# Performance work log

Hardware: AMD Instinct MI355X
Metric: run time of the kernel (lower is better)

The kernel has to match this reference:

```python
import jax, jax.numpy as jnp
import numpy as np

B, S, F, H = 16, 512, 64, 128          # batch, seq_len, price features, lstm hidden
N, GH = 1024, 64                        # graph nodes, graph hidden
FUSE, H1, H2 = 64, 32, 1                # fusion/output head dims


def setup_inputs() -> dict:
    key = jax.random.key(0)
    ks = jax.random.split(key, 24)
    s = 0.05
    inp = {
        'price_sequence': jax.random.normal(ks[0], (B, S, F), jnp.float32),
        'graph_features': jax.random.normal(ks[1], (B, N, 1), jnp.float32),
        'adjacency_mask': (jax.random.uniform(ks[2], (N, N)) > 0.5).astype(jnp.float32),
        # LSTM layer 0 (torch gate order i,f,g,o; weights stored (4H, in))
        'Wih0': jax.random.normal(ks[3], (4 * H, F), jnp.float32) * s,
        'Whh0': jax.random.normal(ks[4], (4 * H, H), jnp.float32) * s,
        'bih0': jnp.zeros((4 * H,), jnp.float32),
        'bhh0': jnp.zeros((4 * H,), jnp.float32),
        # LSTM layer 1
        'Wih1': jax.random.normal(ks[5], (4 * H, H), jnp.float32) * s,
        'Whh1': jax.random.normal(ks[6], (4 * H, H), jnp.float32) * s,
        'bih1': jnp.zeros((4 * H,), jnp.float32),
        'bhh1': jnp.zeros((4 * H,), jnp.float32),
        # graph attention: W: Linear(1, GH) no bias -> (1, GH); attention Linear(2GH,1) split
        'Wg': jax.random.normal(ks[7], (1, GH), jnp.float32) * s,
        'a_src': jax.random.normal(ks[8], (GH,), jnp.float32) * s,
        'a_dst': jax.random.normal(ks[9], (GH,), jnp.float32) * s,
        'adj_w': jax.random.normal(ks[10], (N, N), jnp.float32) * 0.1,
        # fusion + output head
        'Wf': jax.random.normal(ks[11], (H + N * GH, FUSE), jnp.float32) * 0.01,
        'bf': jnp.zeros((FUSE,), jnp.float32),
        'W1': jax.random.normal(ks[12], (FUSE, H1), jnp.float32) * s,
        'b1': jnp.zeros((H1,), jnp.float32),
        'W2': jax.random.normal(ks[13], (H1, H2), jnp.float32) * s,
        'b2': jnp.zeros((H2,), jnp.float32),
    }
    return inp


def _lstm_layer(x, Wih, Whh, bih, bhh):
    # x: (B, S, in) batch_first; returns (B, S, H)
    b = x.shape[0]
    h0 = jnp.zeros((b, Whh.shape[1]), x.dtype)
    c0 = jnp.zeros_like(h0)
    bias = bih + bhh

    def step(carry, xt):
        h, c = carry
        gates = xt @ Wih.T + h @ Whh.T + bias  # (B, 4H)
        i, f, g, o = jnp.split(gates, 4, axis=-1)
        i, f, o = jax.nn.sigmoid(i), jax.nn.sigmoid(f), jax.nn.sigmoid(o)
        g = jnp.tanh(g)
        c = f * c + i * g
        h = o * jnp.tanh(c)
        return (h, c), h

    _, ys = jax.lax.scan(step, (h0, c0), jnp.swapaxes(x, 0, 1))
    return jnp.swapaxes(ys, 0, 1)


def _graph_attention(graph_features, adjacency_mask, Wg, a_src, a_dst, adj_w):
    h = graph_features @ Wg                       # (B, N, GH)
    # Linear([h_i ; h_j]) == h_i@a_src + h_j@a_dst  (decomposed concat-attention)
    e_src = h @ a_src                              # (B, N)
    e_dst = h @ a_dst                              # (B, N)
    scores = e_src[:, :, None] + e_dst[:, None, :]  # (B, N, N)
    scores = scores * adjacency_mask[None]
    scores = scores * jax.nn.sigmoid(adj_w)[None]
    attn = jax.nn.softmax(scores, axis=-1)
    updated = attn @ h                             # (B, N, GH)
    return updated, attn


def reference(price_sequence, graph_features, adjacency_mask,
              Wih0, Whh0, bih0, bhh0, Wih1, Whh1, bih1, bhh1,
              Wg, a_src, a_dst, adj_w, Wf, bf, W1, b1, W2, b2):
    # 2-layer LSTM (eval mode: inter-layer dropout is identity)
    y0 = _lstm_layer(price_sequence, Wih0, Whh0, bih0, bhh0)
    y1 = _lstm_layer(y0, Wih1, Whh1, bih1, bhh1)
    price_repr = y1[:, -1, :]                      # (B, H)

    graph_repr, attn = _graph_attention(graph_features, adjacency_mask, Wg, a_src, a_dst, adj_w)
    graph_flat = graph_repr.reshape(graph_repr.shape[0], -1)  # (B, N*GH)

    combined = jnp.concatenate([price_repr, graph_flat], axis=1)
    fused = jax.nn.relu(combined @ Wf + bf)
    hidden = jax.nn.relu(fused @ W1 + b1)          # head dropout is identity in eval
    predictions = (hidden @ W2 + b2).squeeze(-1)   # (B,)
    return predictions, attn
```

## Files before the change

kernel.cpp:

```cpp
#include <hip/hip_runtime.h>

typedef unsigned int u32;
typedef unsigned long long u64;
typedef _Float16 f16;
typedef _Float16 f16x8 __attribute__((ext_vector_type(8)));
typedef float f32x4 __attribute__((ext_vector_type(4)));

#define DEV __device__ __forceinline__
#define SCP __HIP_MEMORY_SCOPE_AGENT
#define PINA(x) asm volatile("" : "+a"(x))

constexpr size_t O_XG0   = 0;
constexpr size_t O_W0HI  = O_XG0   + 16ull*512*512*4;
constexpr size_t O_W0LO  = O_W0HI  + 512ull*128*2;
constexpr size_t O_WIHHI = O_W0LO  + 512ull*128*2;
constexpr size_t O_WIHLO = O_WIHHI + 512ull*128*2;
constexpr size_t O_WHHHI = O_WIHLO + 512ull*128*2;
constexpr size_t O_WHHLO = O_WHHHI + 512ull*128*2;
constexpr size_t O_B1P   = O_WHHLO + 512ull*128*2;
constexpr size_t O_MSIG  = O_B1P   + 512*4;
constexpr size_t O_ESC   = O_MSIG  + 1024ull*1024*4;
constexpr size_t O_EDST  = O_ESC   + 16384*4;
constexpr size_t O_SBUF  = O_EDST  + 16384*4;
constexpr size_t O_PREPR = O_SBUF  + 16384*4;
constexpr size_t O_WFG   = O_PREPR + 2048*4;
constexpr size_t O_H0HI  = O_WFG   + 65536ull*4;
constexpr size_t O_H0LO  = O_H0HI  + 513ull*16*64*4;
constexpr size_t O_P1    = O_H0LO  + 513ull*16*64*4;
constexpr size_t O_FLG0  = O_P1    + 513ull*16*512*4;
constexpr size_t O_FLGP  = O_FLG0  + 513ull*16*4;

struct U128 { u64 x, y; };
DEV f16x8 asf16x8(u64 a, u64 b){ U128 t; t.x=a; t.y=b; return __builtin_bit_cast(f16x8, t); }
DEV f32x4 asf32x4(u64 a, u64 b){ U128 t; t.x=a; t.y=b; return __builtin_bit_cast(f32x4, t); }
DEV u32 f16bits(f16 v){ return (u32)__builtin_bit_cast(unsigned short, v); }

DEV float sigm(float x){ x = fminf(fmaxf(x,-30.f),30.f); return __builtin_amdgcn_rcpf(1.f + __expf(-x)); }
DEV float tanh_(float x){ x = fminf(fmaxf(x,-15.f),15.f); float t = __expf(2.f*x); return (t-1.f)*__builtin_amdgcn_rcpf(t+1.f); }

DEV u32 FV(int s){ return 0x5AB00000u + (u32)s; }

DEV void spin1(const u32* p, u32 tv){
  int gd = 1<<20;
  while (__hip_atomic_load(p,__ATOMIC_RELAXED,SCP)!=tv && --gd){}
  (void)__hip_atomic_load(p,__ATOMIC_ACQUIRE,SCP);
}

__global__ __launch_bounds__(256) void k_setup(
    const float* __restrict__ price, const float* __restrict__ gf,
    const float* __restrict__ amask, const float* __restrict__ Wih0,
    const float* __restrict__ Whh0, const float* __restrict__ bih0, const float* __restrict__ bhh0,
    const float* __restrict__ Wih1, const float* __restrict__ Whh1,
    const float* __restrict__ bih1, const float* __restrict__ bhh1,
    const float* __restrict__ Wg, const float* __restrict__ a_src, const float* __restrict__ a_dst,
    const float* __restrict__ adj_w, const float* __restrict__ Wf,
    char* __restrict__ ws)
{
  const int tid = threadIdx.x;
  const int jb = blockIdx.x;
  __shared__ float P[16][64];
  __shared__ float Wt[64][128];

  if (jb < 2048) {
    const int tt = jb >> 2, p0 = (jb & 3) * 128;
    float* XG = (float*)(ws + O_XG0);
    { int idx = tid*4; int b = idx>>6, k = idx&63;
      f32x4 v = *(const f32x4*)(price + ((size_t)b*512 + tt)*64 + k);
      *(f32x4*)&P[b][k] = v; }
    { int c = tid>>1, kh = (tid&1)*32;
      int p = p0 + c; int row = (p&3)*128 + (p>>2);
      const float* src = Wih0 + row*64 + kh;
      #pragma unroll
      for (int kk=0; kk<32; kk+=4){ f32x4 v = *(const f32x4*)(src+kk);
        Wt[kh+kk+0][c]=v[0]; Wt[kh+kk+1][c]=v[1]; Wt[kh+kk+2][c]=v[2]; Wt[kh+kk+3][c]=v[3]; } }
    __syncthreads();
    { int c = tid & 127, hh2 = tid >> 7;
      int p = p0 + c; int row = (p&3)*128 + (p>>2);
      float bias = bih0[row] + bhh0[row];
      float acc[8];
      #pragma unroll
      for (int r2=0;r2<8;r2++) acc[r2] = bias;
      for (int k=0;k<64;k++){ float w = Wt[k][c];
        #pragma unroll
        for (int r2=0;r2<8;r2++) acc[r2] += w * P[hh2*8+r2][k]; }
      #pragma unroll
      for (int r2=0;r2<8;r2++)
        XG[((size_t)(hh2*8+r2)*512 + tt)*512 + p0 + c] = acc[r2]; }
  } else if (jb < 3072) {
    int idx = ((jb-2048)<<10) + tid*4;
    float* MS = (float*)(ws + O_MSIG);
    f32x4 m = *(const f32x4*)(amask+idx); f32x4 a = *(const f32x4*)(adj_w+idx);
    f32x4 o;
    #pragma unroll
    for (int e=0;e<4;e++) o[e] = m[e] * (1.f/(1.f+expf(-a[e])));
    *(f32x4*)(MS+idx) = o;
  } else if (jb < 3136) {
    unsigned short* HI = (unsigned short*)(ws+O_W0HI);
    unsigned short* LO = (unsigned short*)(ws+O_W0LO);
    int base = ((jb-3072)*256 + tid)*4;
    #pragma unroll
    for (int e=0;e<4;e++){ int idx = base+e; int p = idx>>7, k = idx&127;
      int row = (p&3)*128 + (p>>2);
      float w = Whh0[row*128 + k];
      f16 hi = (f16)w; f16 lo = (f16)((w - (float)hi)*4096.f);
      HI[idx] = (unsigned short)f16bits(hi); LO[idx] = (unsigned short)f16bits(lo); }
  } else if (jb < 3200) {
    unsigned short* HI = (unsigned short*)(ws+O_WIHHI);
    unsigned short* LO = (unsigned short*)(ws+O_WIHLO);
    int base = ((jb-3136)*256 + tid)*4;
    #pragma unroll
    for (int e=0;e<4;e++){ int idx = base+e; int p = idx>>7, k = idx&127;
      int row = (p&3)*128 + (p>>2);
      float w = Wih1[row*128 + k];
      f16 hi = (f16)w; f16 lo = (f16)((w - (float)hi)*4096.f);
      HI[idx] = (unsigned short)f16bits(hi); LO[idx] = (unsigned short)f16bits(lo); }
  } else if (jb < 3264) {
    unsigned short* HI = (unsigned short*)(ws+O_WHHHI);
    unsigned short* LO = (unsigned short*)(ws+O_WHHLO);
    int base = ((jb-3200)*256 + tid)*4;
    #pragma unroll
    for (int e=0;e<4;e++){ int idx = base+e; int p = idx>>7, k = idx&127;
      int row = (p&3)*128 + (p>>2);
      float w = Whh1[row*128 + k];
      f16 hi = (f16)w; f16 lo = (f16)((w - (float)hi)*4096.f);
      HI[idx] = (unsigned short)f16bits(hi); LO[idx] = (unsigned short)f16bits(lo); }
  } else if (jb < 3265) {
    float* B1 = (float*)(ws+O_B1P);
    for (int p = tid; p < 512; p += 256){ int row = (p&3)*128 + (p>>2); B1[p] = bih1[row]+bhh1[row]; }
  } else if (jb < 3281) {
    float cs = 0.f, cd = 0.f;
    for (int g=0; g<64; g++){ cs += Wg[g]*a_src[g]; cd += Wg[g]*a_dst[g]; }
    float* ESC = (float*)(ws+O_ESC); float* EDS = (float*)(ws+O_EDST);
    int base = (jb-3265)*1024 + tid*4;
    f32x4 g4 = *(const f32x4*)(gf+base);
    f32x4 e1, e2;
    #pragma unroll
    for (int e=0;e<4;e++){ e1[e] = g4[e]*cs; e2[e] = g4[e]*cd; }
    *(f32x4*)(ESC+base) = e1; *(f32x4*)(EDS+base) = e2;
  } else {
    float* WFG = (float*)(ws+O_WFG);
    int n = (jb-3281)*4 + (tid>>6); int f = tid & 63;
    float acc = 0.f;
    for (int g=0; g<64; g++) acc += Wg[g] * Wf[((size_t)(128 + n*64 + g))*64 + f];
    WFG[n*64 + f] = acc;
  }
}

struct SM {
  u32 hHI[2][64];
  u32 hLO[2][64];
  float gbuf[8][64];
  float red[8];
};

template<int LAYER>
DEV void rnn_cu(char* __restrict__ ws, int b, int tid, SM* sm)
{
  const int lane = tid & 63, w = tid >> 6;
  const int c = lane & 15, q = lane >> 4;
  const int j = w*16 + c;

  const u64* WHI = (const u64*)(ws + (LAYER ? O_WHHHI : O_W0HI));
  const u64* WLO = (const u64*)(ws + (LAYER ? O_WHHLO : O_W0LO));
  f16x8 Bhi[4][4], Blo[4][4];
  #pragma unroll
  for (int t=0;t<4;t++)
    #pragma unroll
    for (int ks=0;ks<4;ks++){
      int o = (w*64 + t*16 + c)*32 + ks*8 + q*2;
      Bhi[t][ks] = asf16x8(WHI[o], WHI[o+1]);
      Blo[t][ks] = asf16x8(WLO[o], WLO[o+1]);
    }
  #pragma unroll
  for (int t=0;t<4;t++)
    #pragma unroll
    for (int ks=0;ks<4;ks++){ PINA(Bhi[t][ks]); PINA(Blo[t][ks]); }

  u32* H0HIp = (u32*)(ws+O_H0HI);
  u32* H0LOp = (u32*)(ws+O_H0LO);
  const u64* P1u = (const u64*)(ws+O_P1);
  const u32* FLGPp = (const u32*)(ws+O_FLGP);
  u32* FLG0p = (u32*)(ws+O_FLG0);
  const float* XGb = (const float*)(ws+O_XG0) + (size_t)b*512*512;

  if (q==0 && (c&1)==0){ sm->hHI[0][w*8+(c>>1)] = 0u; sm->hLO[0][w*8+(c>>1)] = 0u; }

  f32x4 xgc = {0,0,0,0}, xgN = {0,0,0,0}, xgNN = {0,0,0,0};
  u64 pc0=0, pc1=0, pn0=0, pn1=0, pnn0=0, pnn1=0;
  if constexpr (!LAYER) {
    xgc = *(const f32x4*)(XGb + 4*j);
    xgN = *(const f32x4*)(XGb + 512 + 4*j);
    xgNN = xgN;
  } else {
    spin1(FLGPp + 1, FV(1));
    { size_t o = ((size_t)(1*16 + b)*512 + 4*j) >> 1;
      pc0 = __hip_atomic_load(P1u+o,   __ATOMIC_RELAXED, SCP);
      pc1 = __hip_atomic_load(P1u+o+1, __ATOMIC_RELAXED, SCP); }
    spin1(FLGPp + 2, FV(2));
    { size_t o = ((size_t)(2*16 + b)*512 + 4*j) >> 1;
      pn0 = __hip_atomic_load(P1u+o,   __ATOMIC_RELAXED, SCP);
      pn1 = __hip_atomic_load(P1u+o+1, __ATOMIC_RELAXED, SCP); }
  }
  u32 huP=0, luP=0;
  float cst = 0.f;
  __syncthreads();
  int cur = 0;

  for (int s=1; s<=512; ++s){
    if constexpr (!LAYER) {
      if (s>=2 && q==0 && (c&1)==0){
        int o = ((s-1)*16 + b)*64 + w*8 + (c>>1);
        __hip_atomic_store(H0HIp+o, huP, __ATOMIC_RELAXED, SCP);
        __hip_atomic_store(H0LOp+o, luP, __ATOMIC_RELAXED, SCP);
      }
      if (s <= 510) xgNN = *(const f32x4*)(XGb + (size_t)(s+1)*512 + 4*j);
    }

    f32x4 acc[4], accl[4];
    #pragma unroll
    for (int t=0;t<4;t++){ acc[t]=f32x4{0,0,0,0}; accl[t]=f32x4{0,0,0,0}; }
    #pragma unroll
    for (int ks=0;ks<4;ks++){
      f16x8 ah  = *(const f16x8*)&sm->hHI[cur][ks*16 + q*4];
      f16x8 al_ = *(const f16x8*)&sm->hLO[cur][ks*16 + q*4];
      #pragma unroll
      for (int t=0;t<4;t++){
        acc[t]  = __builtin_amdgcn_mfma_f32_16x16x32_f16(ah,  Bhi[t][ks], acc[t],  0,0,0);
        accl[t] = __builtin_amdgcn_mfma_f32_16x16x32_f16(ah,  Blo[t][ks], accl[t], 0,0,0);
        accl[t] = __builtin_amdgcn_mfma_f32_16x16x32_f16(al_, Bhi[t][ks], accl[t], 0,0,0);
      }
    }

    if constexpr (LAYER) {
      if (s+2 <= 512){
        spin1(FLGPp + (s+2), FV(s+2));
        size_t o = ((size_t)((s+2)*16 + b)*512 + 4*j) >> 1;
        pnn0 = __hip_atomic_load(P1u+o,   __ATOMIC_RELAXED, SCP);
        pnn1 = __hip_atomic_load(P1u+o+1, __ATOMIC_RELAXED, SCP);
      }
    }

    if (q==0){
      #pragma unroll
      for (int t=0;t<4;t++) sm->gbuf[w][t*16+c] = acc[t][0] + accl[t][0]*(1.f/4096.f);
    }
    f32x4 g4 = *(const f32x4*)&sm->gbuf[w][4*c];
    f32x4 add = LAYER ? asf32x4(pc0,pc1) : xgc;
    float I = sigm(g4[0]+add[0]);
    float F = sigm(g4[1]+add[1]);
    float G = tanh_(g4[2]+add[2]);
    float O = sigm(g4[3]+add[3]);
    cst = F*cst + I*G;
    float hv = O * tanh_(cst);

    f16 hh = (f16)hv; f16 hl = (f16)((hv - (float)hh)*4096.f);
    u32 hb = f16bits(hh), lb = f16bits(hl);
    u32 oh = (u32)__shfl_xor((int)hb, 1, 64);
    u32 ol = (u32)__shfl_xor((int)lb, 1, 64);
    u32 hu = hb | (oh<<16), lu = lb | (ol<<16);
    int nxt = cur^1;
    if (q==0 && (c&1)==0){ sm->hHI[nxt][w*8+(c>>1)] = hu; sm->hLO[nxt][w*8+(c>>1)] = lu; }
    if constexpr (LAYER){ if (s==512 && q==0) ((float*)(ws+O_PREPR))[b*128 + j] = hv; }

    if constexpr (!LAYER){ asm volatile("s_waitcnt vmcnt(0)" ::: "memory"); }
    __syncthreads();
    if constexpr (!LAYER){
      if (s>=2 && tid==0)
        __hip_atomic_store(FLG0p + (s-1)*16 + b, FV(s-1), __ATOMIC_RELAXED, SCP);
    }
    huP=hu; luP=lu; cur = nxt;
    xgc = xgN; xgN = xgNN;
    pc0=pn0; pc1=pn1; pn0=pnn0; pn1=pnn1;
  }

  if constexpr (!LAYER){
    if (q==0 && (c&1)==0){
      int o = (512*16 + b)*64 + w*8 + (c>>1);
      __hip_atomic_store(H0HIp+o, huP, __ATOMIC_RELAXED, SCP);
      __hip_atomic_store(H0LOp+o, luP, __ATOMIC_RELAXED, SCP);
    }
    asm volatile("s_waitcnt vmcnt(0)" ::: "memory");
    __syncthreads();
    if (tid==0) __hip_atomic_store(FLG0p + 512*16 + b, FV(512), __ATOMIC_RELAXED, SCP);
  }
}

DEV void gemm_cu(char* __restrict__ ws, int g, int tid)
{
  const int lane = tid & 63, w = tid >> 6;
  const int c = lane & 15, q = lane >> 4;

  const u64* WHI = (const u64*)(ws+O_WIHHI);
  const u64* WLO = (const u64*)(ws+O_WIHLO);
  f16x8 Bhi[4][4], Blo[4][4];
  #pragma unroll
  for (int t=0;t<4;t++)
    #pragma unroll
    for (int ks=0;ks<4;ks++){
      int o = (w*64 + t*16 + c)*32 + ks*8 + q*2;
      Bhi[t][ks] = asf16x8(WHI[o], WHI[o+1]);
      Blo[t][ks] = asf16x8(WLO[o], WLO[o+1]);
    }
  #pragma unroll
  for (int t=0;t<4;t++)
    #pragma unroll
    for (int ks=0;ks<4;ks++){ PINA(Bhi[t][ks]); PINA(Blo[t][ks]); }

  float bias_t[4];
  #pragma unroll
  for (int t=0;t<4;t++) bias_t[t] = ((const float*)(ws+O_B1P))[w*64 + t*16 + c];

  const u64* H0HIu = (const u64*)(ws+O_H0HI);
  const u64* H0LOu = (const u64*)(ws+O_H0LO);
  const u32* FLG0p = (const u32*)(ws+O_FLG0);
  u32* FLGPp = (u32*)(ws+O_FLGP);
  float* P1f = (float*)(ws+O_P1);

  for (int s = 1+g; s <= 512; s += 3){
    { const u32* fp = FLG0p + s*16 + c; int gd = 1<<20; u32 tv = FV(s);
      for(;;){ bool ok = (lane>=16) || (__hip_atomic_load(fp,__ATOMIC_RELAXED,SCP)==tv);
               if (__all(ok) || !--gd) break; }
      (void)__hip_atomic_load(fp, __ATOMIC_ACQUIRE, SCP); }

    u64 AH[4][2], AL[4][2];
    #pragma unroll
    for (int ks=0;ks<4;ks++){
      size_t o = ((size_t)(s*16 + c))*32 + ks*8 + q*2;
      AH[ks][0]=__hip_atomic_load(H0HIu+o,  __ATOMIC_RELAXED,SCP);
      AH[ks][1]=__hip_atomic_load(H0HIu+o+1,__ATOMIC_RELAXED,SCP);
      AL[ks][0]=__hip_atomic_load(H0LOu+o,  __ATOMIC_RELAXED,SCP);
      AL[ks][1]=__hip_atomic_load(H0LOu+o+1,__ATOMIC_RELAXED,SCP);
    }
    f32x4 acc[4], accl[4];
    #pragma unroll
    for (int t=0;t<4;t++){ acc[t]=f32x4{0,0,0,0}; accl[t]=f32x4{0,0,0,0}; }
    #pragma unroll
    for (int ks=0;ks<4;ks++){
      f16x8 ah  = asf16x8(AH[ks][0], AH[ks][1]);
      f16x8 al_ = asf16x8(AL[ks][0], AL[ks][1]);
      #pragma unroll
      for (int t=0;t<4;t++){
        acc[t]  = __builtin_amdgcn_mfma_f32_16x16x32_f16(ah,  Bhi[t][ks], acc[t],  0,0,0);
        accl[t] = __builtin_amdgcn_mfma_f32_16x16x32_f16(ah,  Blo[t][ks], accl[t], 0,0,0);
        accl[t] = __builtin_amdgcn_mfma_f32_16x16x32_f16(al_, Bhi[t][ks], accl[t], 0,0,0);
      }
    }
    #pragma unroll
    for (int t=0;t<4;t++){
      #pragma unroll
      for (int i=0;i<4;i++){
        float v = acc[t][i] + accl[t][i]*(1.f/4096.f) + bias_t[t];
        __hip_atomic_store(P1f + ((size_t)(s*16 + q*4 + i))*512 + w*64 + t*16 + c,
                           v, __ATOMIC_RELAXED, SCP);
      }
    }
    asm volatile("s_waitcnt vmcnt(0)" ::: "memory");
    __syncthreads();
    if (tid==0) __hip_atomic_store(FLGPp + s, FV(s), __ATOMIC_RELAXED, SCP);
  }
}

DEV float wredMax(float v){
  #pragma unroll
  for (int o=32;o;o>>=1) v = fmaxf(v, __shfl_xor(v,o,64));
  return v;
}
DEV float wredSum(float v){
  #pragma unroll
  for (int o=32;o;o>>=1) v += __shfl_xor(v,o,64);
  return v;
}

__global__
__attribute__((amdgpu_flat_work_group_size(512,512), amdgpu_waves_per_eu(2,2)))
void k_main(const float* __restrict__ gf, char* __restrict__ ws, float* __restrict__ out)
{
  __shared__ SM sm;
  const int tid = threadIdx.x;
  const int bid = blockIdx.x;

  if (bid < 16) { rnn_cu<0>(ws, bid, tid, &sm); return; }
  if (bid < 32) { rnn_cu<1>(ws, bid-16, tid, &sm); return; }
  if (bid < 35) { gemm_cu(ws, bid-32, tid); return; }

  const int row = bid - 35;
  const int b = row >> 10, i = row & 1023;
  const int w = tid >> 6;
  const float* MSIG = (const float*)(ws+O_MSIG);
  const float* ESC  = (const float*)(ws+O_ESC);
  const float* EDST = (const float*)(ws+O_EDST);
  float* SBUF = (float*)(ws+O_SBUF);

  const float ei = ESC[(b<<10)+i];
  float pv[2];
  float mx = -3.4e38f;
  #pragma unroll
  for (int k2=0;k2<2;k2++){
    int jj = tid + (k2<<9);
    float sc = (ei + EDST[(b<<10)+jj]) * MSIG[((size_t)i<<10)+jj];
    pv[k2] = sc; mx = fmaxf(mx, sc);
  }
  mx = wredMax(mx);
  if ((tid&63)==0) sm.red[w] = mx;
  __syncthreads();
  mx = fmaxf(fmaxf(fmaxf(sm.red[0],sm.red[1]),fmaxf(sm.red[2],sm.red[3])),
             fmaxf(fmaxf(sm.red[4],sm.red[5]),fmaxf(sm.red[6],sm.red[7])));
  __syncthreads();

  float sum = 0.f;
  #pragma unroll
  for (int k2=0;k2<2;k2++){ pv[k2] = __expf(pv[k2]-mx); sum += pv[k2]; }
  sum = wredSum(sum);
  if ((tid&63)==0) sm.red[w] = sum;
  __syncthreads();
  sum = sm.red[0]+sm.red[1]+sm.red[2]+sm.red[3]+sm.red[4]+sm.red[5]+sm.red[6]+sm.red[7];
  __syncthreads();

  const float rinv = 1.0f / sum;
  float sacc = 0.f;
  const size_t obase = 16 + ((size_t)row << 10);
  #pragma unroll
  for (int k2=0;k2<2;k2++){
    int jj = tid + (k2<<9);
    float a = pv[k2]*rinv;
    out[obase + jj] = a;
    sacc += a * gf[(b<<10)+jj];
  }
  sacc = wredSum(sacc);
  if ((tid&63)==0) sm.red[w] = sacc;
  __syncthreads();
  if (tid==0) SBUF[row] = sm.red[0]+sm.red[1]+sm.red[2]+sm.red[3]
                        + sm.red[4]+sm.red[5]+sm.red[6]+sm.red[7];
}

__global__ __launch_bounds__(256) void k_mlp(const float* __restrict__ Wf, const float* __restrict__ bf,
  const float* __restrict__ W1, const float* __restrict__ b1,
  const float* __restrict__ W2, const float* __restrict__ b2,
  const char* __restrict__ ws, float* __restrict__ out)
{
  __shared__ float sS[1024];
  __shared__ float sP[128];
  __shared__ float sR[256];
  __shared__ float sF[96];
  const int b = blockIdx.x, tid = threadIdx.x;
  const float* SBUF = (const float*)(ws+O_SBUF);
  const float* PREPR= (const float*)(ws+O_PREPR);
  const float* WFG  = (const float*)(ws+O_WFG);

  { f32x4 v = *(const f32x4*)(SBUF + (b<<10) + tid*4); *(f32x4*)&sS[tid*4] = v; }
  if (tid < 128) sP[tid] = PREPR[b*128 + tid];
  __syncthreads();

  const int f = tid & 63, kq = tid >> 6;
  float acc = 0.f;
  for (int n = kq*256; n < kq*256+256; ++n) acc += sS[n] * WFG[n*64 + f];
  if (kq == 0) {
    for (int k=0;k<128;k++) acc += sP[k] * Wf[k*64 + f];
    acc += bf[f];
  }
  sR[tid] = acc; __syncthreads();
  if (tid < 64) {
    float v = sR[tid] + sR[tid+64] + sR[tid+128] + sR[tid+192];
    sF[tid] = fmaxf(v, 0.f);
  }
  __syncthreads();
  if (tid < 32) {
    float a = 0.f;
    for (int k=0;k<64;k++) a += sF[k] * W1[k*32 + tid];
    sF[64+tid] = fmaxf(a + b1[tid], 0.f);
  }
  __syncthreads();
  if (tid == 0) {
    float a = 0.f;
    for (int k=0;k<32;k++) a += sF[64+k] * W2[k];
    out[b] = a + b2[0];
  }
}

extern "C" void kernel_launch(void* const* d_in, const int* in_sizes, int n_in,
                              void* d_out, int out_size, void* d_ws, size_t ws_size,
                              hipStream_t stream)
{
  const float* price = (const float*)d_in[0];
  const float* gf    = (const float*)d_in[1];
  const float* amask = (const float*)d_in[2];
  const float* Wih0  = (const float*)d_in[3];
  const float* Whh0  = (const float*)d_in[4];
  const float* bih0  = (const float*)d_in[5];
  const float* bhh0  = (const float*)d_in[6];
  const float* Wih1  = (const float*)d_in[7];
  const float* Whh1  = (const float*)d_in[8];
  const float* bih1  = (const float*)d_in[9];
  const float* bhh1  = (const float*)d_in[10];
  const float* Wg    = (const float*)d_in[11];
  const float* asrc  = (const float*)d_in[12];
  const float* adst  = (const float*)d_in[13];
  const float* adjw  = (const float*)d_in[14];
  const float* Wf    = (const float*)d_in[15];
  const float* bf    = (const float*)d_in[16];
  const float* W1    = (const float*)d_in[17];
  const float* b1    = (const float*)d_in[18];
  const float* W2    = (const float*)d_in[19];
  const float* b2    = (const float*)d_in[20];
  char* ws = (char*)d_ws;
  float* out = (float*)d_out;

  k_setup<<<dim3(3537), dim3(256), 0, stream>>>(price, gf, amask, Wih0, Whh0, bih0, bhh0,
                                                Wih1, Whh1, bih1, bhh1, Wg, asrc, adst, adjw, Wf, ws);
  k_main<<<dim3(35 + 16384), dim3(512), 0, stream>>>(gf, ws, out);
  k_mlp<<<dim3(16), dim3(256), 0, stream>>>(Wf, bf, W1, b1, W2, b2, (const char*)ws, out);
}
```

Baseline: 1.205 ms.

## Replace flag-synchronized LSTM layer pipeline with separate sequential kernel launches

Splits the single persistent kernel into separate launches: layer-0 recurrence plus attention rows, a batched input-projection GEMM over all timesteps, then the layer-1 recurrence. This removes the global flag spinning and the per-step vmcnt waits, and uses an LDS-only barrier in the recurrent loop. The cost is that the two recurrences no longer overlap, so their serial step chains add up.

```diff
diff --git a/kernel.cpp b/kernel.cpp
--- a/kernel.cpp
+++ b/kernel.cpp
@@ -27,8 +27,6 @@
 constexpr size_t O_H0HI  = O_WFG   + 65536ull*4;
 constexpr size_t O_H0LO  = O_H0HI  + 513ull*16*64*4;
 constexpr size_t O_P1    = O_H0LO  + 513ull*16*64*4;
-constexpr size_t O_FLG0  = O_P1    + 513ull*16*512*4;
-constexpr size_t O_FLGP  = O_FLG0  + 513ull*16*4;
 
 struct U128 { u64 x, y; };
 DEV f16x8 asf16x8(u64 a, u64 b){ U128 t; t.x=a; t.y=b; return __builtin_bit_cast(f16x8, t); }
@@ -38,12 +36,10 @@
 DEV float sigm(float x){ x = fminf(fmaxf(x,-30.f),30.f); return __builtin_amdgcn_rcpf(1.f + __expf(-x)); }
 DEV float tanh_(float x){ x = fminf(fmaxf(x,-15.f),15.f); float t = __expf(2.f*x); return (t-1.f)*__builtin_amdgcn_rcpf(t+1.f); }
 
-DEV u32 FV(int s){ return 0x5AB00000u + (u32)s; }
-
-DEV void spin1(const u32* p, u32 tv){
-  int gd = 1<<20;
-  while (__hip_atomic_load(p,__ATOMIC_RELAXED,SCP)!=tv && --gd){}
-  (void)__hip_atomic_load(p,__ATOMIC_ACQUIRE,SCP);
+DEV void bar_lds(){
+  asm volatile("s_waitcnt lgkmcnt(0)" ::: "memory");
+  __builtin_amdgcn_s_barrier();
+  __builtin_amdgcn_sched_barrier(0);
 }
 
 __global__ __launch_bounds__(256) void k_setup(
@@ -154,7 +150,7 @@
 };
 
 template<int LAYER>
-DEV void rnn_cu(char* __restrict__ ws, int b, int tid, SM* sm)
+DEV void rnn_seq(char* __restrict__ ws, int b, int tid, SM* sm)
 {
   const int lane = tid & 63, w = tid >> 6;
   const int c = lane & 15, q = lane >> 4;
@@ -179,8 +175,6 @@
   u32* H0HIp = (u32*)(ws+O_H0HI);
   u32* H0LOp = (u32*)(ws+O_H0LO);
   const u64* P1u = (const u64*)(ws+O_P1);
-  const u32* FLGPp = (const u32*)(ws+O_FLGP);
-  u32* FLG0p = (u32*)(ws+O_FLG0);
   const float* XGb = (const float*)(ws+O_XG0) + (size_t)b*512*512;
 
   if (q==0 && (c&1)==0){ sm->hHI[0][w*8+(c>>1)] = 0u; sm->hLO[0][w*8+(c>>1)] = 0u; }
@@ -190,21 +184,18 @@
   if constexpr (!LAYER) {
     xgc = *(const f32x4*)(XGb + 4*j);
     xgN = *(const f32x4*)(XGb + 512 + 4*j);
-    xgNN = xgN;
   } else {
-    spin1(FLGPp + 1, FV(1));
     { size_t o = ((size_t)(1*16 + b)*512 + 4*j) >> 1;
       pc0 = __hip_atomic_load(P1u+o,   __ATOMIC_RELAXED, SCP);
       pc1 = __hip_atomic_load(P1u+o+1, __ATOMIC_RELAXED, SCP); }
-    spin1(FLGPp + 2, FV(2));
     { size_t o = ((size_t)(2*16 + b)*512 + 4*j) >> 1;
       pn0 = __hip_atomic_load(P1u+o,   __ATOMIC_RELAXED, SCP);
       pn1 = __hip_atomic_load(P1u+o+1, __ATOMIC_RELAXED, SCP); }
   }
   u32 huP=0, luP=0;
   float cst = 0.f;
-  __syncthreads();
   int cur = 0;
+  __syncthreads();
 
   for (int s=1; s<=512; ++s){
     if constexpr (!LAYER) {
@@ -214,6 +205,12 @@
         __hip_atomic_store(H0LOp+o, luP, __ATOMIC_RELAXED, SCP);
       }
       if (s <= 510) xgNN = *(const f32x4*)(XGb + (size_t)(s+1)*512 + 4*j);
+    } else {
+      if (s+2 <= 512){
+        size_t o = ((size_t)((s+2)*16 + b)*512 + 4*j) >> 1;
+        pnn0 = __hip_atomic_load(P1u+o,   __ATOMIC_RELAXED, SCP);
+        pnn1 = __hip_atomic_load(P1u+o+1, __ATOMIC_RELAXED, SCP);
+      }
     }
 
     f32x4 acc[4], accl[4];
@@ -231,15 +228,6 @@
       }
     }
 
-    if constexpr (LAYER) {
-      if (s+2 <= 512){
-        spin1(FLGPp + (s+2), FV(s+2));
-        size_t o = ((size_t)((s+2)*16 + b)*512 + 4*j) >> 1;
-        pnn0 = __hip_atomic_load(P1u+o,   __ATOMIC_RELAXED, SCP);
-        pnn1 = __hip_atomic_load(P1u+o+1, __ATOMIC_RELAXED, SCP);
-      }
-    }
-
     if (q==0){
       #pragma unroll
       for (int t=0;t<4;t++) sm->gbuf[w][t*16+c] = acc[t][0] + accl[t][0]*(1.f/4096.f);
@@ -262,12 +250,8 @@
     if (q==0 && (c&1)==0){ sm->hHI[nxt][w*8+(c>>1)] = hu; sm->hLO[nxt][w*8+(c>>1)] = lu; }
     if constexpr (LAYER){ if (s==512 && q==0) ((float*)(ws+O_PREPR))[b*128 + j] = hv; }
 
-    if constexpr (!LAYER){ asm volatile("s_waitcnt vmcnt(0)" ::: "memory"); }
-    __syncthreads();
-    if constexpr (!LAYER){
-      if (s>=2 && tid==0)
-        __hip_atomic_store(FLG0p + (s-1)*16 + b, FV(s-1), __ATOMIC_RELAXED, SCP);
-    }
+    bar_lds();
+
     huP=hu; luP=lu; cur = nxt;
     xgc = xgN; xgN = xgNN;
     pc0=pn0; pc1=pn1; pn0=pnn0; pn1=pnn1;
@@ -279,84 +263,6 @@
       __hip_atomic_store(H0HIp+o, huP, __ATOMIC_RELAXED, SCP);
       __hip_atomic_store(H0LOp+o, luP, __ATOMIC_RELAXED, SCP);
     }
-    asm volatile("s_waitcnt vmcnt(0)" ::: "memory");
-    __syncthreads();
-    if (tid==0) __hip_atomic_store(FLG0p + 512*16 + b, FV(512), __ATOMIC_RELAXED, SCP);
-  }
-}
-
-DEV void gemm_cu(char* __restrict__ ws, int g, int tid)
-{
-  const int lane = tid & 63, w = tid >> 6;
-  const int c = lane & 15, q = lane >> 4;
-
-  const u64* WHI = (const u64*)(ws+O_WIHHI);
-  const u64* WLO = (const u64*)(ws+O_WIHLO);
-  f16x8 Bhi[4][4], Blo[4][4];
-  #pragma unroll
-  for (int t=0;t<4;t++)
-    #pragma unroll
-    for (int ks=0;ks<4;ks++){
-      int o = (w*64 + t*16 + c)*32 + ks*8 + q*2;
-      Bhi[t][ks] = asf16x8(WHI[o], WHI[o+1]);
-      Blo[t][ks] = asf16x8(WLO[o], WLO[o+1]);
-    }
-  #pragma unroll
-  for (int t=0;t<4;t++)
-    #pragma unroll
-    for (int ks=0;ks<4;ks++){ PINA(Bhi[t][ks]); PINA(Blo[t][ks]); }
-
-  float bias_t[4];
-  #pragma unroll
-  for (int t=0;t<4;t++) bias_t[t] = ((const float*)(ws+O_B1P))[w*64 + t*16 + c];
-
-  const u64* H0HIu = (const u64*)(ws+O_H0HI);
-  const u64* H0LOu = (const u64*)(ws+O_H0LO);
-  const u32* FLG0p = (const u32*)(ws+O_FLG0);
-  u32* FLGPp = (u32*)(ws+O_FLGP);
-  float* P1f = (float*)(ws+O_P1);
-
-  for (int s = 1+g; s <= 512; s += 3){
-    { const u32* fp = FLG0p + s*16 + c; int gd = 1<<20; u32 tv = FV(s);
-      for(;;){ bool ok = (lane>=16) || (__hip_atomic_load(fp,__ATOMIC_RELAXED,SCP)==tv);
-               if (__all(ok) || !--gd) break; }
-      (void)__hip_atomic_load(fp, __ATOMIC_ACQUIRE, SCP); }
-
-    u64 AH[4][2], AL[4][2];
-    #pragma unroll
-    for (int ks=0;ks<4;ks++){
-      size_t o = ((size_t)(s*16 + c))*32 + ks*8 + q*2;
-      AH[ks][0]=__hip_atomic_load(H0HIu+o,  __ATOMIC_RELAXED,SCP);
-      AH[ks][1]=__hip_atomic_load(H0HIu+o+1,__ATOMIC_RELAXED,SCP);
-      AL[ks][0]=__hip_atomic_load(H0LOu+o,  __ATOMIC_RELAXED,SCP);
-      AL[ks][1]=__hip_atomic_load(H0LOu+o+1,__ATOMIC_RELAXED,SCP);
-    }
-    f32x4 acc[4], accl[4];
-    #pragma unroll
-    for (int t=0;t<4;t++){ acc[t]=f32x4{0,0,0,0}; accl[t]=f32x4{0,0,0,0}; }
-    #pragma unroll
-    for (int ks=0;ks<4;ks++){
-      f16x8 ah  = asf16x8(AH[ks][0], AH[ks][1]);
-      f16x8 al_ = asf16x8(AL[ks][0], AL[ks][1]);
-      #pragma unroll
-      for (int t=0;t<4;t++){
-        acc[t]  = __builtin_amdgcn_mfma_f32_16x16x32_f16(ah,  Bhi[t][ks], acc[t],  0,0,0);
-        accl[t] = __builtin_amdgcn_mfma_f32_16x16x32_f16(ah,  Blo[t][ks], accl[t], 0,0,0);
-        accl[t] = __builtin_amdgcn_mfma_f32_16x16x32_f16(al_, Bhi[t][ks], accl[t], 0,0,0);
-      }
-    }
-    #pragma unroll
-    for (int t=0;t<4;t++){
-      #pragma unroll
-      for (int i=0;i<4;i++){
-        float v = acc[t][i] + accl[t][i]*(1.f/4096.f) + bias_t[t];
-        __hip_atomic_store(P1f + ((size_t)(s*16 + q*4 + i))*512 + w*64 + t*16 + c,
-                           v, __ATOMIC_RELAXED, SCP);
-      }
-    }
-    asm volatile("s_waitcnt vmcnt(0)" ::: "memory");
-    __syncthreads();
-    if (tid==0) __hip_atomic_store(FLGPp + s, FV(s), __ATOMIC_RELAXED, SCP);
   }
 }
 
@@ -373,17 +279,15 @@
 
 __global__
 __attribute__((amdgpu_flat_work_group_size(512,512), amdgpu_waves_per_eu(2,2)))
-void k_main(const float* __restrict__ gf, char* __restrict__ ws, float* __restrict__ out)
+void k_lstm0(const float* __restrict__ gf, char* __restrict__ ws, float* __restrict__ out)
 {
   __shared__ SM sm;
   const int tid = threadIdx.x;
   const int bid = blockIdx.x;
 
-  if (bid < 16) { rnn_cu<0>(ws, bid, tid, &sm); return; }
-  if (bid < 32) { rnn_cu<1>(ws, bid-16, tid, &sm); return; }
-  if (bid < 35) { gemm_cu(ws, bid-32, tid); return; }
-
-  const int row = bid - 35;
+  if (bid < 16) { rnn_seq<0>(ws, bid, tid, &sm); return; }
+
+  const int row = bid - 16;
   const int b = row >> 10, i = row & 1023;
   const int w = tid >> 6;
   const float* MSIG = (const float*)(ws+O_MSIG);
@@ -431,6 +335,75 @@
   __syncthreads();
   if (tid==0) SBUF[row] = sm.red[0]+sm.red[1]+sm.red[2]+sm.red[3]
                         + sm.red[4]+sm.red[5]+sm.red[6]+sm.red[7];
+}
+
+__global__
+__attribute__((amdgpu_flat_work_group_size(512,512), amdgpu_waves_per_eu(2,2)))
+void k_gemm1(char* __restrict__ ws)
+{
+  const int tid = threadIdx.x;
+  const int lane = tid & 63, w = tid >> 6;
+  const int c = lane & 15, q = lane >> 4;
+  const int s = blockIdx.x + 1;
+
+  const u64* WHI = (const u64*)(ws+O_WIHHI);
+  const u64* WLO = (const u64*)(ws+O_WIHLO);
+  f16x8 Bhi[4][4], Blo[4][4];
+  #pragma unroll
+  for (int t=0;t<4;t++)
+    #pragma unroll
+    for (int ks=0;ks<4;ks++){
+      int o = (w*64 + t*16 + c)*32 + ks*8 + q*2;
+      Bhi[t][ks] = asf16x8(WHI[o], WHI[o+1]);
+      Blo[t][ks] = asf16x8(WLO[o], WLO[o+1]);
+    }
+  float bias_t[4];
+  #pragma unroll
+  for (int t=0;t<4;t++) bias_t[t] = ((const float*)(ws+O_B1P))[w*64 + t*16 + c];
+
+  const u64* H0HIu = (const u64*)(ws+O_H0HI);
+  const u64* H0LOu = (const u64*)(ws+O_H0LO);
+  float* P1f = (float*)(ws+O_P1);
+
+  u64 AH[4][2], AL[4][2];
+  #pragma unroll
+  for (int ks=0;ks<4;ks++){
+    size_t o = ((size_t)(s*16 + c))*32 + ks*8 + q*2;
+    AH[ks][0]=__hip_atomic_load(H0HIu+o,  __ATOMIC_RELAXED,SCP);
+    AH[ks][1]=__hip_atomic_load(H0HIu+o+1,__ATOMIC_RELAXED,SCP);
+    AL[ks][0]=__hip_atomic_load(H0LOu+o,  __ATOMIC_RELAXED,SCP);
+    AL[ks][1]=__hip_atomic_load(H0LOu+o+1,__ATOMIC_RELAXED,SCP);
+  }
+  f32x4 acc[4], accl[4];
+  #pragma unroll
+  for (int t=0;t<4;t++){ acc[t]=f32x4{0,0,0,0}; accl[t]=f32x4{0,0,0,0}; }
+  #pragma unroll
+  for (int ks=0;ks<4;ks++){
+    f16x8 ah  = asf16x8(AH[ks][0], AH[ks][1]);
+    f16x8 al_ = asf16x8(AL[ks][0], AL[ks][1]);
+    #pragma unroll
+    for (int t=0;t<4;t++){
+      acc[t]  = __builtin_amdgcn_mfma_f32_16x16x32_f16(ah,  Bhi[t][ks], acc[t],  0,0,0);
+      accl[t] = __builtin_amdgcn_mfma_f32_16x16x32_f16(ah,  Blo[t][ks], accl[t], 0,0,0);
+      accl[t] = __builtin_amdgcn_mfma_f32_16x16x32_f16(al_, Bhi[t][ks], accl[t], 0,0,0);
+    }
+  }
+  #pragma unroll
+  for (int t=0;t<4;t++){
+    #pragma unroll
+    for (int i=0;i<4;i++){
+      float v = acc[t][i] + accl[t][i]*(1.f/4096.f) + bias_t[t];
+      P1f[((size_t)(s*16 + q*4 + i))*512 + w*64 + t*16 + c] = v;
+    }
+  }
+}
+
+__global__
+__attribute__((amdgpu_flat_work_group_size(512,512), amdgpu_waves_per_eu(2,2)))
+void k_lstm1(char* __restrict__ ws)
+{
+  __shared__ SM sm;
+  rnn_seq<1>(ws, blockIdx.x, threadIdx.x, &sm);
 }
 
 __global__ __launch_bounds__(256) void k_mlp(const float* __restrict__ Wf, const float* __restrict__ bf,
@@ -507,6 +480,8 @@
 
   k_setup<<<dim3(3537), dim3(256), 0, stream>>>(price, gf, amask, Wih0, Whh0, bih0, bhh0,
                                                 Wih1, Whh1, bih1, bhh1, Wg, asrc, adst, adjw, Wf, ws);
-  k_main<<<dim3(35 + 16384), dim3(512), 0, stream>>>(gf, ws, out);
+  k_lstm0<<<dim3(16 + 16384), dim3(512), 0, stream>>>(gf, ws, out);
+  k_gemm1<<<dim3(512), dim3(512), 0, stream>>>(ws);
+  k_lstm1<<<dim3(16), dim3(512), 0, stream>>>(ws);
   k_mlp<<<dim3(16), dim3(256), 0, stream>>>(Wf, bf, W1, b1, W2, b2, (const char*)ws, out);
 }
```

Result: slower. 1.554 ms (+28.9%).

## Batch eight sequences per recurrent workgroup and split attention into its own kernel

Applied to the files above, without the earlier changes.

The recurrent LSTM workgroups now each handle eight batch rows instead of one, using the MFMA M dimension (hi and lo f16 halves of h stacked as 16 rows), so only 2+2 recurrent blocks run instead of 16+16. Gate outputs are regathered through a padded LDS transpose, and the error-correction term uses a cross-lane shuffle. The graph-attention rows move into a separate kernel launched after the recurrent one, and the flag layout changes to per-group strides. This cuts per-step MFMA waste and barrier count per sequence, but each block does more serial work per step and attention no longer overlaps with the recurrence.

```diff
diff --git a/kernel.cpp b/kernel.cpp
--- a/kernel.cpp
+++ b/kernel.cpp
@@ -32,7 +32,6 @@
 
 struct U128 { u64 x, y; };
 DEV f16x8 asf16x8(u64 a, u64 b){ U128 t; t.x=a; t.y=b; return __builtin_bit_cast(f16x8, t); }
-DEV f32x4 asf32x4(u64 a, u64 b){ U128 t; t.x=a; t.y=b; return __builtin_bit_cast(f32x4, t); }
 DEV u32 f16bits(f16 v){ return (u32)__builtin_bit_cast(unsigned short, v); }
 
 DEV float sigm(float x){ x = fminf(fmaxf(x,-30.f),30.f); return __builtin_amdgcn_rcpf(1.f + __expf(-x)); }
@@ -44,6 +43,17 @@
   int gd = 1<<20;
   while (__hip_atomic_load(p,__ATOMIC_RELAXED,SCP)!=tv && --gd){}
   (void)__hip_atomic_load(p,__ATOMIC_ACQUIRE,SCP);
+}
+
+DEV void bar_lds(){
+  asm volatile("s_waitcnt lgkmcnt(0)" ::: "memory");
+  __builtin_amdgcn_s_barrier();
+  __builtin_amdgcn_sched_barrier(0);
+}
+DEV void bar_vm2(){
+  asm volatile("s_waitcnt vmcnt(2) lgkmcnt(0)" ::: "memory");
+  __builtin_amdgcn_s_barrier();
+  __builtin_amdgcn_sched_barrier(0);
 }
 
 __global__ __launch_bounds__(256) void k_setup(
@@ -146,19 +156,18 @@
   }
 }
 
-struct SM {
-  u32 hHI[2][64];
-  u32 hLO[2][64];
-  float gbuf[8][64];
-  float red[8];
+struct SM2 {
+  u32 hbuf[2][16][72];
+  float gbuf[8][585];
 };
 
 template<int LAYER>
-DEV void rnn_cu(char* __restrict__ ws, int b, int tid, SM* sm)
+DEV void rnn2(char* __restrict__ ws, int bg, int tid, SM2* sm)
 {
   const int lane = tid & 63, w = tid >> 6;
-  const int c = lane & 15, q = lane >> 4;
-  const int j = w*16 + c;
+  const int r = lane & 15, q = lane >> 4;
+  const int b_loc = lane >> 3, jl0 = lane & 7;
+  const int B = bg*8 + b_loc;
 
   const u64* WHI = (const u64*)(ws + (LAYER ? O_WHHHI : O_W0HI));
   const u64* WLO = (const u64*)(ws + (LAYER ? O_WHHLO : O_W0LO));
@@ -167,7 +176,7 @@
   for (int t=0;t<4;t++)
     #pragma unroll
     for (int ks=0;ks<4;ks++){
-      int o = (w*64 + t*16 + c)*32 + ks*8 + q*2;
+      int o = (w*64 + t*16 + r)*32 + ks*8 + q*2;
       Bhi[t][ks] = asf16x8(WHI[o], WHI[o+1]);
       Blo[t][ks] = asf16x8(WLO[o], WLO[o+1]);
     }
@@ -178,110 +187,174 @@
 
   u32* H0HIp = (u32*)(ws+O_H0HI);
   u32* H0LOp = (u32*)(ws+O_H0LO);
-  const u64* P1u = (const u64*)(ws+O_P1);
+  const float* P1f = (const float*)(ws+O_P1);
   const u32* FLGPp = (const u32*)(ws+O_FLGP);
   u32* FLG0p = (u32*)(ws+O_FLG0);
-  const float* XGb = (const float*)(ws+O_XG0) + (size_t)b*512*512;
-
-  if (q==0 && (c&1)==0){ sm->hHI[0][w*8+(c>>1)] = 0u; sm->hLO[0][w*8+(c>>1)] = 0u; }
-
-  f32x4 xgc = {0,0,0,0}, xgN = {0,0,0,0}, xgNN = {0,0,0,0};
-  u64 pc0=0, pc1=0, pn0=0, pn1=0, pnn0=0, pnn1=0;
+  const float* XGb = (const float*)(ws+O_XG0) + (size_t)B*512*512;
+
+  for (int idx = tid; idx < 2*16*72; idx += 512) ((u32*)sm->hbuf)[idx] = 0u;
+
+  f32x4 xgc[2], xgN[2], xgNN[2];
+  f32x4 p1c[2], p1n[2], p1nn[2];
+  #pragma unroll
+  for (int g2=0; g2<2; ++g2){ xgc[g2]=f32x4{0,0,0,0}; xgN[g2]=f32x4{0,0,0,0}; xgNN[g2]=f32x4{0,0,0,0};
+                              p1c[g2]=f32x4{0,0,0,0}; p1n[g2]=f32x4{0,0,0,0}; p1nn[g2]=f32x4{0,0,0,0}; }
   if constexpr (!LAYER) {
-    xgc = *(const f32x4*)(XGb + 4*j);
-    xgN = *(const f32x4*)(XGb + 512 + 4*j);
-    xgNN = xgN;
+    #pragma unroll
+    for (int g2=0; g2<2; ++g2){
+      int jg = 16*w + 8*g2 + jl0;
+      xgc[g2] = *(const f32x4*)(XGb + 4*jg);
+      xgN[g2] = *(const f32x4*)(XGb + 512 + 4*jg);
+    }
   } else {
-    spin1(FLGPp + 1, FV(1));
-    { size_t o = ((size_t)(1*16 + b)*512 + 4*j) >> 1;
-      pc0 = __hip_atomic_load(P1u+o,   __ATOMIC_RELAXED, SCP);
-      pc1 = __hip_atomic_load(P1u+o+1, __ATOMIC_RELAXED, SCP); }
-    spin1(FLGPp + 2, FV(2));
-    { size_t o = ((size_t)(2*16 + b)*512 + 4*j) >> 1;
-      pn0 = __hip_atomic_load(P1u+o,   __ATOMIC_RELAXED, SCP);
-      pn1 = __hip_atomic_load(P1u+o+1, __ATOMIC_RELAXED, SCP); }
-  }
-  u32 huP=0, luP=0;
-  float cst = 0.f;
-  __syncthreads();
+    spin1(FLGPp + 1*16, FV(1));
+    #pragma unroll
+    for (int g2=0; g2<2; ++g2){
+      int jg = 16*w + 8*g2 + jl0;
+      p1c[g2] = *(const f32x4*)(P1f + ((size_t)(1*16 + B))*512 + 4*jg);
+    }
+    spin1(FLGPp + 2*16, FV(2));
+    #pragma unroll
+    for (int g2=0; g2<2; ++g2){
+      int jg = 16*w + 8*g2 + jl0;
+      p1n[g2] = *(const f32x4*)(P1f + ((size_t)(2*16 + B))*512 + 4*jg);
+    }
+  }
+  u32 huP[2] = {0,0}, luP[2] = {0,0};
+  float cst[2] = {0.f, 0.f};
   int cur = 0;
+  __syncthreads();
 
   for (int s=1; s<=512; ++s){
     if constexpr (!LAYER) {
-      if (s>=2 && q==0 && (c&1)==0){
-        int o = ((s-1)*16 + b)*64 + w*8 + (c>>1);
-        __hip_atomic_store(H0HIp+o, huP, __ATOMIC_RELAXED, SCP);
-        __hip_atomic_store(H0LOp+o, luP, __ATOMIC_RELAXED, SCP);
-      }
-      if (s <= 510) xgNN = *(const f32x4*)(XGb + (size_t)(s+1)*512 + 4*j);
-    }
-
-    f32x4 acc[4], accl[4];
-    #pragma unroll
-    for (int t=0;t<4;t++){ acc[t]=f32x4{0,0,0,0}; accl[t]=f32x4{0,0,0,0}; }
+      if (s>=2 && (jl0&1)==0){
+        #pragma unroll
+        for (int g2=0; g2<2; ++g2){
+          int o = ((s-1)*16 + B)*64 + 8*w + 4*g2 + (jl0>>1);
+          __hip_atomic_store(H0HIp+o, huP[g2], __ATOMIC_RELAXED, SCP);
+          __hip_atomic_store(H0LOp+o, luP[g2], __ATOMIC_RELAXED, SCP);
+        }
+      }
+      __builtin_amdgcn_sched_barrier(0);
+      { int rowN = (s<=510) ? (s+1) : 511;
+        #pragma unroll
+        for (int g2=0; g2<2; ++g2){
+          int jg = 16*w + 8*g2 + jl0;
+          xgNN[g2] = *(const f32x4*)(XGb + (size_t)rowN*512 + 4*jg);
+        } }
+    }
+
+    f32x4 accA[4], accB[4];
+    #pragma unroll
+    for (int t=0;t<4;t++){ accA[t]=f32x4{0,0,0,0}; accB[t]=f32x4{0,0,0,0}; }
     #pragma unroll
     for (int ks=0;ks<4;ks++){
-      f16x8 ah  = *(const f16x8*)&sm->hHI[cur][ks*16 + q*4];
-      f16x8 al_ = *(const f16x8*)&sm->hLO[cur][ks*16 + q*4];
+      f16x8 av = *(const f16x8*)&sm->hbuf[cur][r][ks*16 + q*4];
       #pragma unroll
       for (int t=0;t<4;t++){
-        acc[t]  = __builtin_amdgcn_mfma_f32_16x16x32_f16(ah,  Bhi[t][ks], acc[t],  0,0,0);
-        accl[t] = __builtin_amdgcn_mfma_f32_16x16x32_f16(ah,  Blo[t][ks], accl[t], 0,0,0);
-        accl[t] = __builtin_amdgcn_mfma_f32_16x16x32_f16(al_, Bhi[t][ks], accl[t], 0,0,0);
+        accA[t] = __builtin_amdgcn_mfma_f32_16x16x32_f16(av, Bhi[t][ks], accA[t], 0,0,0);
+        accB[t] = __builtin_amdgcn_mfma_f32_16x16x32_f16(av, Blo[t][ks], accB[t], 0,0,0);
       }
     }
 
     if constexpr (LAYER) {
       if (s+2 <= 512){
-        spin1(FLGPp + (s+2), FV(s+2));
-        size_t o = ((size_t)((s+2)*16 + b)*512 + 4*j) >> 1;
-        pnn0 = __hip_atomic_load(P1u+o,   __ATOMIC_RELAXED, SCP);
-        pnn1 = __hip_atomic_load(P1u+o+1, __ATOMIC_RELAXED, SCP);
-      }
-    }
-
-    if (q==0){
-      #pragma unroll
-      for (int t=0;t<4;t++) sm->gbuf[w][t*16+c] = acc[t][0] + accl[t][0]*(1.f/4096.f);
-    }
-    f32x4 g4 = *(const f32x4*)&sm->gbuf[w][4*c];
-    f32x4 add = LAYER ? asf32x4(pc0,pc1) : xgc;
-    float I = sigm(g4[0]+add[0]);
-    float F = sigm(g4[1]+add[1]);
-    float G = tanh_(g4[2]+add[2]);
-    float O = sigm(g4[3]+add[3]);
-    cst = F*cst + I*G;
-    float hv = O * tanh_(cst);
-
-    f16 hh = (f16)hv; f16 hl = (f16)((hv - (float)hh)*4096.f);
-    u32 hb = f16bits(hh), lb = f16bits(hl);
-    u32 oh = (u32)__shfl_xor((int)hb, 1, 64);
-    u32 ol = (u32)__shfl_xor((int)lb, 1, 64);
-    u32 hu = hb | (oh<<16), lu = lb | (ol<<16);
+        spin1(FLGPp + (s+2)*16, FV(s+2));
+        #pragma unroll
+        for (int g2=0; g2<2; ++g2){
+          int jg = 16*w + 8*g2 + jl0;
+          p1nn[g2] = *(const f32x4*)(P1f + ((size_t)((s+2)*16 + B))*512 + 4*jg);
+        }
+      }
+    }
+
+    f32x4 gate_t[4];
+    #pragma unroll
+    for (int t=0;t<4;t++){
+      #pragma unroll
+      for (int i=0;i<4;i++){
+        float corr = __shfl_xor(accA[t][i], 32, 64);
+        gate_t[t][i] = accA[t][i] + (corr + accB[t][i])*(1.f/4096.f);
+      }
+    }
+    if (q < 2){
+      #pragma unroll
+      for (int t=0;t<4;t++)
+        *(f32x4*)&sm->gbuf[w][(t*16 + r)*9 + q*4] = gate_t[t];
+    }
+
+    float hv2[2];
+    #pragma unroll
+    for (int g2=0; g2<2; ++g2){
+      int jgl = jl0 + 8*g2;
+      int t = jgl>>2, cb = (jgl&3)*4;
+      float g0 = sm->gbuf[w][(t*16+cb+0)*9 + b_loc];
+      float g1 = sm->gbuf[w][(t*16+cb+1)*9 + b_loc];
+      float g2v= sm->gbuf[w][(t*16+cb+2)*9 + b_loc];
+      float g3 = sm->gbuf[w][(t*16+cb+3)*9 + b_loc];
+      f32x4 add = LAYER ? p1c[g2] : xgc[g2];
+      float I = sigm(g0+add[0]);
+      float F = sigm(g1+add[1]);
+      float G = tanh_(g2v+add[2]);
+      float O = sigm(g3+add[3]);
+      cst[g2] = F*cst[g2] + I*G;
+      hv2[g2] = O * tanh_(cst[g2]);
+    }
+
+    u32 HU[2], LU[2];
+    #pragma unroll
+    for (int g2=0; g2<2; ++g2){
+      f16 hh = (f16)hv2[g2]; f16 hl = (f16)((hv2[g2] - (float)hh)*4096.f);
+      u32 hb = f16bits(hh), lb = f16bits(hl);
+      u32 oh = (u32)__shfl_xor((int)hb, 1, 64);
+      u32 ol = (u32)__shfl_xor((int)lb, 1, 64);
+      HU[g2] = hb | (oh<<16); LU[g2] = lb | (ol<<16);
+    }
     int nxt = cur^1;
-    if (q==0 && (c&1)==0){ sm->hHI[nxt][w*8+(c>>1)] = hu; sm->hLO[nxt][w*8+(c>>1)] = lu; }
-    if constexpr (LAYER){ if (s==512 && q==0) ((float*)(ws+O_PREPR))[b*128 + j] = hv; }
-
-    if constexpr (!LAYER){ asm volatile("s_waitcnt vmcnt(0)" ::: "memory"); }
-    __syncthreads();
+    if ((jl0&1)==0){
+      #pragma unroll
+      for (int g2=0; g2<2; ++g2){
+        int jp = 8*w + 4*g2 + (jl0>>1);
+        sm->hbuf[nxt][b_loc][jp]   = HU[g2];
+        sm->hbuf[nxt][b_loc+8][jp] = LU[g2];
+      }
+    }
+    if constexpr (LAYER){
+      if (s==512){
+        #pragma unroll
+        for (int g2=0; g2<2; ++g2)
+          ((float*)(ws+O_PREPR))[B*128 + 16*w + 8*g2 + jl0] = hv2[g2];
+      }
+    }
+
     if constexpr (!LAYER){
+      bar_vm2();
       if (s>=2 && tid==0)
-        __hip_atomic_store(FLG0p + (s-1)*16 + b, FV(s-1), __ATOMIC_RELAXED, SCP);
-    }
-    huP=hu; luP=lu; cur = nxt;
-    xgc = xgN; xgN = xgNN;
-    pc0=pn0; pc1=pn1; pn0=pnn0; pn1=pnn1;
+        __hip_atomic_store(FLG0p + (s-1)*16 + bg, FV(s-1), __ATOMIC_RELAXED, SCP);
+    } else {
+      bar_lds();
+    }
+    huP[0]=HU[0]; huP[1]=HU[1]; luP[0]=LU[0]; luP[1]=LU[1];
+    cur = nxt;
+    #pragma unroll
+    for (int g2=0; g2<2; ++g2){
+      xgc[g2]=xgN[g2]; xgN[g2]=xgNN[g2];
+      p1c[g2]=p1n[g2]; p1n[g2]=p1nn[g2];
+    }
   }
 
   if constexpr (!LAYER){
-    if (q==0 && (c&1)==0){
-      int o = (512*16 + b)*64 + w*8 + (c>>1);
-      __hip_atomic_store(H0HIp+o, huP, __ATOMIC_RELAXED, SCP);
-      __hip_atomic_store(H0LOp+o, luP, __ATOMIC_RELAXED, SCP);
+    if ((jl0&1)==0){
+      #pragma unroll
+      for (int g2=0; g2<2; ++g2){
+        int o = (512*16 + B)*64 + 8*w + 4*g2 + (jl0>>1);
+        __hip_atomic_store(H0HIp+o, huP[g2], __ATOMIC_RELAXED, SCP);
+        __hip_atomic_store(H0LOp+o, luP[g2], __ATOMIC_RELAXED, SCP);
+      }
     }
     asm volatile("s_waitcnt vmcnt(0)" ::: "memory");
     __syncthreads();
-    if (tid==0) __hip_atomic_store(FLG0p + 512*16 + b, FV(512), __ATOMIC_RELAXED, SCP);
+    if (tid==0) __hip_atomic_store(FLG0p + 512*16 + bg, FV(512), __ATOMIC_RELAXED, SCP);
   }
 }
 
@@ -317,8 +390,8 @@
   float* P1f = (float*)(ws+O_P1);
 
   for (int s = 1+g; s <= 512; s += 3){
-    { const u32* fp = FLG0p + s*16 + c; int gd = 1<<20; u32 tv = FV(s);
-      for(;;){ bool ok = (lane>=16) || (__hip_atomic_load(fp,__ATOMIC_RELAXED,SCP)==tv);
+    { const u32* fp = FLG0p + s*16 + (lane&15); int gd = 1<<20; u32 tv = FV(s);
+      for(;;){ bool ok = ((lane&15)>=2) || (__hip_atomic_load(fp,__ATOMIC_RELAXED,SCP)==tv);
                if (__all(ok) || !--gd) break; }
       (void)__hip_atomic_load(fp, __ATOMIC_ACQUIRE, SCP); }
 
@@ -356,8 +429,20 @@
     }
     asm volatile("s_waitcnt vmcnt(0)" ::: "memory");
     __syncthreads();
-    if (tid==0) __hip_atomic_store(FLGPp + s, FV(s), __ATOMIC_RELAXED, SCP);
-  }
+    if (tid==0) __hip_atomic_store(FLGPp + s*16, FV(s), __ATOMIC_RELAXED, SCP);
+  }
+}
+
+__global__
+__attribute__((amdgpu_flat_work_group_size(512,512), amdgpu_waves_per_eu(2,2)))
+void k_main(char* __restrict__ ws)
+{
+  __shared__ SM2 sm;
+  const int tid = threadIdx.x;
+  const int bid = blockIdx.x;
+  if (bid < 2)      rnn2<0>(ws, bid, tid, &sm);
+  else if (bid < 5) gemm_cu(ws, bid-2, tid);
+  else              rnn2<1>(ws, bid-5, tid, &sm);
 }
 
 DEV float wredMax(float v){
@@ -371,19 +456,12 @@
   return v;
 }
 
-__global__
-__attribute__((amdgpu_flat_work_group_size(512,512), amdgpu_waves_per_eu(2,2)))
-void k_main(const float* __restrict__ gf, char* __restrict__ ws, float* __restrict__ out)
-{
-  __shared__ SM sm;
+__global__ __launch_bounds__(512) void k_attn(const float* __restrict__ gf,
+                                              char* __restrict__ ws, float* __restrict__ out)
+{
+  __shared__ float red[8];
   const int tid = threadIdx.x;
-  const int bid = blockIdx.x;
-
-  if (bid < 16) { rnn_cu<0>(ws, bid, tid, &sm); return; }
-  if (bid < 32) { rnn_cu<1>(ws, bid-16, tid, &sm); return; }
-  if (bid < 35) { gemm_cu(ws, bid-32, tid); return; }
-
-  const int row = bid - 35;
+  const int row = blockIdx.x;
   const int b = row >> 10, i = row & 1023;
   const int w = tid >> 6;
   const float* MSIG = (const float*)(ws+O_MSIG);
@@ -401,19 +479,19 @@
     pv[k2] = sc; mx = fmaxf(mx, sc);
   }
   mx = wredMax(mx);
-  if ((tid&63)==0) sm.red[w] = mx;
-  __syncthreads();
-  mx = fmaxf(fmaxf(fmaxf(sm.red[0],sm.red[1]),fmaxf(sm.red[2],sm.red[3])),
-             fmaxf(fmaxf(sm.red[4],sm.red[5]),fmaxf(sm.red[6],sm.red[7])));
+  if ((tid&63)==0) red[w] = mx;
+  __syncthreads();
+  mx = fmaxf(fmaxf(fmaxf(red[0],red[1]),fmaxf(red[2],red[3])),
+             fmaxf(fmaxf(red[4],red[5]),fmaxf(red[6],red[7])));
   __syncthreads();
 
   float sum = 0.f;
   #pragma unroll
   for (int k2=0;k2<2;k2++){ pv[k2] = __expf(pv[k2]-mx); sum += pv[k2]; }
   sum = wredSum(sum);
-  if ((tid&63)==0) sm.red[w] = sum;
-  __syncthreads();
-  sum = sm.red[0]+sm.red[1]+sm.red[2]+sm.red[3]+sm.red[4]+sm.red[5]+sm.red[6]+sm.red[7];
+  if ((tid&63)==0) red[w] = sum;
+  __syncthreads();
+  sum = red[0]+red[1]+red[2]+red[3]+red[4]+red[5]+red[6]+red[7];
   __syncthreads();
 
   const float rinv = 1.0f / sum;
@@ -427,10 +505,9 @@
     sacc += a * gf[(b<<10)+jj];
   }
   sacc = wredSum(sacc);
-  if ((tid&63)==0) sm.red[w] = sacc;
-  __syncthreads();
-  if (tid==0) SBUF[row] = sm.red[0]+sm.red[1]+sm.red[2]+sm.red[3]
-                        + sm.red[4]+sm.red[5]+sm.red[6]+sm.red[7];
+  if ((tid&63)==0) red[w] = sacc;
+  __syncthreads();
+  if (tid==0) SBUF[row] = red[0]+red[1]+red[2]+red[3]+red[4]+red[5]+red[6]+red[7];
 }
 
 __global__ __launch_bounds__(256) void k_mlp(const float* __restrict__ Wf, const float* __restrict__ bf,
@@ -507,6 +584,7 @@
 
   k_setup<<<dim3(3537), dim3(256), 0, stream>>>(price, gf, amask, Wih0, Whh0, bih0, bhh0,
                                                 Wih1, Whh1, bih1, bhh1, Wg, asrc, adst, adjw, Wf, ws);
-  k_main<<<dim3(35 + 16384), dim3(512), 0, stream>>>(gf, ws, out);
+  k_main<<<dim3(7), dim3(512), 0, stream>>>(ws);
+  k_attn<<<dim3(16384), dim3(512), 0, stream>>>(gf, ws, out);
   k_mlp<<<dim3(16), dim3(256), 0, stream>>>(Wf, bf, W1, b1, W2, b2, (const char*)ws, out);
 }
```

After: 1.409 ms. 16.9% more time.
